# Kernel optimization log

Measured on AMD Instinct MI355X. Metric: run time of the kernel, lower is better.

## Reference

```python
import jax, jax.numpy as jnp
import numpy as np

EPS = 1e-5
M = 8          # num_modules
NUM_LAYERS = 4


def gumbel_softmax(logits, u, tau):
    g = -jnp.log(-jnp.log(jnp.clip(u, 1e-10, 1.0 - 1e-7)))
    return jax.nn.softmax((logits + g) / tau, axis=-1)


def batchnorm(x, gamma, beta):
    # training-mode BN over batch axis 0; x: [B, ...], gamma/beta broadcast over trailing dims
    mean = jnp.mean(x, axis=0, keepdims=True)
    var = jnp.mean(jnp.square(x - mean), axis=0, keepdims=True)  # biased var, as torch BN
    return (x - mean) * jax.lax.rsqrt(var + EPS) * gamma + beta


def setup_inputs() -> dict:
    key = jax.random.key(0)
    ks = jax.random.split(key, 32)
    B = 16384
    d = {}
    d['x'] = jax.random.normal(ks[0], (B, 128), jnp.float32)
    d['embedding_input'] = jax.random.normal(ks[1], (B, 128), jnp.float32)
    d['u_sel'] = jax.random.uniform(ks[2], (B, NUM_LAYERS - 1, M, M), jnp.float32)
    d['u_final'] = jax.random.uniform(ks[3], (B, M), jnp.float32)
    shapes = [('base_W0', (128, 400)), ('base_b0', (400,)), ('base_W1', (400, 256)), ('base_b1', (256,)),
              ('em_W0', (128, 400)), ('em_b0', (400,)),
              ('gat_W0', (400, 256)), ('gat_b0', (256,)), ('gat_W1', (256, 256)), ('gat_b1', (256,)),
              ('sel_W', (3, 256, 64)), ('sel_b', (3, 64)), ('selF_W', (256, 8)), ('selF_b', (8,)),
              ('cond_W', (3, 64, 256)), ('cond_b', (3, 256)),
              ('mod_W', (8, 256, 256)), ('mod_b', (8, 256)),
              ('last_W', (256, 18)), ('last_b', (18,))]
    for i, (name, sh) in enumerate(shapes):
        fan_in = sh[-2] if len(sh) >= 2 else sh[-1]
        d[name] = jax.random.normal(ks[4 + i], sh, jnp.float32) / np.sqrt(fan_in)
    d['bn1_g'] = jnp.ones((8, 256), jnp.float32)
    d['bn1_b'] = jnp.zeros((8, 256), jnp.float32)
    d['bn2_g'] = jnp.ones((8, 256), jnp.float32)
    d['bn2_b'] = jnp.zeros((8, 256), jnp.float32)
    return d


def forward(x, embedding_input, u_sel, u_final,
            base_W0, base_b0, base_W1, base_b1, em_W0, em_b0,
            gat_W0, gat_b0, gat_W1, gat_b1,
            sel_W, sel_b, selF_W, selF_b, cond_W, cond_b,
            mod_W, mod_b, bn1_g, bn1_b, bn2_g, bn2_b, last_W, last_b):
    relu = jax.nn.relu
    # base MLP (last activation is identity)
    h = relu(x @ base_W0 + base_b0)
    out = h @ base_W1 + base_b1                       # [B, 256]
    # embedding base (single layer, identity last activation)
    emb = embedding_input @ em_W0 + em_b0             # [B, 400]
    # gating fcs: activation THEN fc, per source loop
    emb = relu(emb) @ gat_W0 + gat_b0
    emb = relu(emb) @ gat_W1 + gat_b1                 # [B, 256]

    # routing logits (stochastic branch, tau = select_temp = 1.0)
    select_input = relu(emb)
    gsels = []
    for i in range(NUM_LAYERS - 1):
        logit = jnp.tanh(select_input @ sel_W[i] + sel_b[i])       # [B, 64]
        sraw = logit.reshape(logit.shape[0], M, M)                  # [B, M, M]
        gsels.append(gumbel_softmax(sraw, u_sel[:, i], 1.0))
        select_input = relu((logit @ cond_W[i] + cond_b[i]) * emb)
    final_select = gumbel_softmax(select_input @ selF_W + selF_b, u_final, 1.0)  # [B, M]
    # selects were insert(0, ...)'d in torch -> consumed in reversed order
    selects = gsels[::-1]

    # layer-0 expert modules: BN -> Linear -> BN (only layers[0] is used in forward)
    mean = jnp.mean(out, axis=0, keepdims=True)
    var = jnp.mean(jnp.square(out - mean), axis=0, keepdims=True)
    xhat = (out - mean) * jax.lax.rsqrt(var + EPS)                  # shared normalization
    t = xhat[:, None, :] * bn1_g + bn1_b                            # [B, M, 256] per-module affine
    h = jnp.einsum('bmd,mdh->bmh', t, mod_W) + mod_b                # [B, M, 256]
    prev = batchnorm(h, bn2_g, bn2_b)                               # [B, M, 256]

    # cascade: weighted combination + relu per layer
    for l in range(NUM_LAYERS - 1):
        prev = relu(jnp.einsum('bmk,bkh->bmh', selects[l], prev))
    out = jnp.einsum('bm,bmh->bh', final_select, prev)              # [B, 256]
    return out @ last_W + last_b                                    # [B, 18]


def reference(x, embedding_input, u_sel, u_final,
              base_W0, base_b0, base_W1, base_b1, em_W0, em_b0,
              gat_W0, gat_b0, gat_W1, gat_b1,
              sel_W, sel_b, selF_W, selF_b, cond_W, cond_b,
              mod_W, mod_b, bn1_g, bn1_b, bn2_g, bn2_b, last_W, last_b):
    return forward(x, embedding_input, u_sel, u_final,
                   base_W0, base_b0, base_W1, base_b1, em_W0, em_b0,
                   gat_W0, gat_b0, gat_W1, gat_b1,
                   sel_W, sel_b, selF_W, selF_b, cond_W, cond_b,
                   mod_W, mod_b, bn1_g, bn1_b, bn2_g, bn2_b, last_W, last_b)
```

## Files before the change

kernel.cpp:

```cpp
#include <hip/hip_runtime.h>
#include <math.h>


#define EPI_NONE  0
#define EPI_RELU  1
#define EPI_TANH  2
#define EPI_COND  3
#define EPI_STATS 4

typedef short bf16x8 __attribute__((ext_vector_type(8)));
typedef float f32x4 __attribute__((ext_vector_type(4)));

__device__ __forceinline__ unsigned short f2bf(float f) {
  unsigned u = __float_as_uint(f);
  u += 0x7fffu + ((u >> 16) & 1u);
  return (unsigned short)(u >> 16);
}
__device__ __forceinline__ float bf2f(unsigned short h) {
  return __uint_as_float(((unsigned)h) << 16);
}
__device__ __forceinline__ void gload_lds16(const void* g, void* l) {
  __builtin_amdgcn_global_load_lds(
      (const __attribute__((address_space(1))) unsigned int*)g,
      (__attribute__((address_space(3))) unsigned int*)l, 16, 0, 0);
}
__device__ __forceinline__ bf16x8 relu_bf8(bf16x8 v) {
  bf16x8 r;
  #pragma unroll
  for (int j = 0; j < 8; ++j) r[j] = v[j] > 0 ? v[j] : (short)0;
  return r;
}

__global__ __launch_bounds__(256) void prep_all(
    const float* __restrict__ x, const float* __restrict__ embi,
    const float* __restrict__ base_W0, const float* __restrict__ em_W0,
    const float* __restrict__ base_W1, const float* __restrict__ gat_W0,
    const float* __restrict__ gat_W1, const float* __restrict__ sel_W,
    const float* __restrict__ cond_W, const float* __restrict__ last_W,
    unsigned short* __restrict__ x_bf, unsigned short* __restrict__ e_bf,
    unsigned short* __restrict__ W0t, unsigned short* __restrict__ emW0t,
    unsigned short* __restrict__ W1t, unsigned short* __restrict__ g0t,
    unsigned short* __restrict__ g1t, unsigned short* __restrict__ selWt,
    unsigned short* __restrict__ condWt, unsigned short* __restrict__ lastWt,
    float* __restrict__ stats)
{
  __shared__ float t[32][33];
  int bid = blockIdx.x;
  const int tid = threadIdx.x;

  if (bid < 4096) {
    const float* src = bid < 2048 ? x : embi;
    unsigned short* dst = bid < 2048 ? x_bf : e_bf;
    const int i = ((bid & 2047) * 256 + tid) * 4;
    const float4 v = *reinterpret_cast<const float4*>(&src[i]);
    ushort4 o;
    o.x = f2bf(v.x); o.y = f2bf(v.y); o.z = f2bf(v.z); o.w = f2bf(v.w);
    *reinterpret_cast<ushort4*>(&dst[i]) = o;
    return;
  }
  bid -= 4096;

  const int tx = tid & 31, ty = tid >> 5;

  if (bid < 496) {
    const float* src; unsigned short* dst; int K, N, KP, gx, local;
    if (bid < 64)       { src = base_W0; dst = W0t;   K = 128; N = 400; KP = 128; gx = 4;  local = bid; }
    else if (bid < 128) { src = em_W0;   dst = emW0t; K = 128; N = 400; KP = 128; gx = 4;  local = bid - 64; }
    else if (bid < 232) { src = base_W1; dst = W1t;   K = 400; N = 256; KP = 416; gx = 13; local = bid - 128; }
    else if (bid < 336) { src = gat_W0;  dst = g0t;   K = 400; N = 256; KP = 416; gx = 13; local = bid - 232; }
    else if (bid < 400) { src = gat_W1;  dst = g1t;   K = 256; N = 256; KP = 256; gx = 8;  local = bid - 336; }
    else if (bid < 448) {
      const int i = (bid - 400) / 16;
      src = sel_W + i * 16384; dst = selWt + i * 16384;
      K = 256; N = 64; KP = 256; gx = 8; local = (bid - 400) % 16;
    } else {
      const int i = (bid - 448) / 16;
      src = cond_W + i * 16384; dst = condWt + i * 16384;
      K = 64; N = 256; KP = 64; gx = 2; local = (bid - 448) % 16;
    }
    const int k0 = (local % gx) * 32, n0 = (local / gx) * 32;
    #pragma unroll
    for (int p = 0; p < 4; ++p) {
      const int k = k0 + ty + p * 8;
      t[ty + p * 8][tx] = (k < K && n0 + tx < N) ? src[(size_t)k * N + n0 + tx] : 0.f;
    }
    __syncthreads();
    #pragma unroll
    for (int p = 0; p < 4; ++p) {
      const int n = n0 + ty + p * 8;
      dst[(size_t)n * KP + k0 + tx] = f2bf(t[tx][ty + p * 8]);
    }
    return;
  }
  bid -= 496;

  if (bid < 8) {
    const int k0 = bid * 32;
    #pragma unroll
    for (int p = 0; p < 4; ++p)
      t[ty + p * 8][tx] = (tx < 18) ? last_W[(size_t)(k0 + ty + p * 8) * 18 + tx] : 0.f;
    __syncthreads();
    #pragma unroll
    for (int p = 0; p < 4; ++p) {
      const int n = ty + p * 8;
      lastWt[(size_t)n * 256 + k0 + tx] = f2bf(t[tx][n]);
      lastWt[(size_t)(n + 32) * 256 + k0 + tx] = 0;
    }
    return;
  }

  for (int i = tid; i < 4608; i += 256) stats[i] = 0.f;
}

template<int BN, int WM, int WN, int EPI, bool RELU_A>
__global__ __launch_bounds__(256) void gemm_bf16(
    const unsigned short* __restrict__ A, int AS,
    const unsigned short* __restrict__ Wt, const float* __restrict__ bias,
    unsigned short* __restrict__ C, int CS, int Nreal, int NP, int K,
    const unsigned short* __restrict__ emb,
    float* __restrict__ sum, float* __restrict__ sumsq)
{
  constexpr int FRAG_M = 128 / WM / 16;
  constexpr int FRAG_N = BN / WN / 16;
  __shared__ unsigned short As[128 * 32];
  __shared__ unsigned short Bs[BN * 32];
  const int row0 = blockIdx.y * 128;
  const int n0 = blockIdx.x * BN;
  const int tid = threadIdx.x;
  const int wid = tid >> 6, lane = tid & 63;
  const int wr = wid / WN, wc = wid % WN;
  const int arow = tid >> 2;
  const int kcol = (tid & 3) * 8;
  const int lr = lane & 15, lk = (lane >> 4) * 8;
  const int lrow = (lane >> 4) * 4;

  f32x4 acc[FRAG_M][FRAG_N] = {};
  for (int k0 = 0; k0 < K; k0 += 32) {
    gload_lds16(A + (size_t)(row0 + arow) * AS + k0 + kcol, (char*)As + tid * 16);
    gload_lds16(A + (size_t)(row0 + 64 + arow) * AS + k0 + kcol, (char*)As + 4096 + tid * 16);
    gload_lds16(Wt + (size_t)(n0 + arow) * K + k0 + kcol, (char*)Bs + tid * 16);
    if constexpr (BN == 128)
      gload_lds16(Wt + (size_t)(n0 + 64 + arow) * K + k0 + kcol, (char*)Bs + 4096 + tid * 16);
    __syncthreads();
    bf16x8 a[FRAG_M], b[FRAG_N];
    #pragma unroll
    for (int i = 0; i < FRAG_M; ++i) {
      a[i] = *reinterpret_cast<const bf16x8*>(&As[(wr * (128 / WM) + i * 16 + lr) * 32 + lk]);
      if (RELU_A) a[i] = relu_bf8(a[i]);
    }
    #pragma unroll
    for (int j = 0; j < FRAG_N; ++j)
      b[j] = *reinterpret_cast<const bf16x8*>(&Bs[(wc * (BN / WN) + j * 16 + lr) * 32 + lk]);
    #pragma unroll
    for (int i = 0; i < FRAG_M; ++i)
      #pragma unroll
      for (int j = 0; j < FRAG_N; ++j)
        acc[i][j] = __builtin_amdgcn_mfma_f32_16x16x32_bf16(a[i], b[j], acc[i][j], 0, 0, 0);
    __syncthreads();
  }
  #pragma unroll
  for (int j = 0; j < FRAG_N; ++j) {
    const int col = n0 + wc * (BN / WN) + j * 16 + lr;
    if (col >= NP) continue;
    const bool real = col < Nreal;
    const float bv = real ? bias[col] : 0.f;
    float s = 0.f, q = 0.f;
    #pragma unroll
    for (int i = 0; i < FRAG_M; ++i) {
      #pragma unroll
      for (int r = 0; r < 4; ++r) {
        const int row = row0 + wr * (128 / WM) + i * 16 + lrow + r;
        float v = acc[i][j][r] + bv;
        if (EPI == EPI_RELU) v = fmaxf(v, 0.f);
        if (EPI == EPI_TANH) v = tanhf(v);
        if (EPI == EPI_COND) { v *= bf2f(emb[(size_t)row * 256 + col]); v = fmaxf(v, 0.f); }
        if (!real) v = 0.f;
        const unsigned short hv = f2bf(v);
        C[(size_t)row * CS + col] = hv;
        if (EPI == EPI_STATS) {
          const float vr = bf2f(hv);
          s += vr;
          q = fmaf(vr, vr, q);
        }
      }
    }
    if (EPI == EPI_STATS) {
      s += __shfl_xor(s, 16); s += __shfl_xor(s, 32);
      q += __shfl_xor(q, 16); q += __shfl_xor(q, 32);
      if (lane < 16) {
        atomicAdd(&sum[col], s);
        atomicAdd(&sumsq[col], q);
      }
    }
  }
}

__global__ __launch_bounds__(256) void gemm_last(
    const unsigned short* __restrict__ A, const unsigned short* __restrict__ Wt,
    const float* __restrict__ bias, float* __restrict__ out)
{
  __shared__ unsigned short As[128 * 32];
  __shared__ unsigned short Bs[64 * 32];
  const int row0 = blockIdx.y * 128;
  const int tid = threadIdx.x;
  const int wid = tid >> 6, lane = tid & 63;
  const int arow = tid >> 2;
  const int kcol = (tid & 3) * 8;
  const int lr = lane & 15, lk = (lane >> 4) * 8;
  const int lrow = (lane >> 4) * 4;

  f32x4 acc[2][4] = {};
  for (int k0 = 0; k0 < 256; k0 += 32) {
    gload_lds16(A + (size_t)(row0 + arow) * 256 + k0 + kcol, (char*)As + tid * 16);
    gload_lds16(A + (size_t)(row0 + 64 + arow) * 256 + k0 + kcol, (char*)As + 4096 + tid * 16);
    gload_lds16(Wt + (size_t)arow * 256 + k0 + kcol, (char*)Bs + tid * 16);
    __syncthreads();
    bf16x8 a[2], b[4];
    #pragma unroll
    for (int i = 0; i < 2; ++i)
      a[i] = *reinterpret_cast<const bf16x8*>(&As[(wid * 32 + i * 16 + lr) * 32 + lk]);
    #pragma unroll
    for (int j = 0; j < 4; ++j)
      b[j] = *reinterpret_cast<const bf16x8*>(&Bs[(j * 16 + lr) * 32 + lk]);
    #pragma unroll
    for (int i = 0; i < 2; ++i)
      #pragma unroll
      for (int j = 0; j < 4; ++j)
        acc[i][j] = __builtin_amdgcn_mfma_f32_16x16x32_bf16(a[i], b[j], acc[i][j], 0, 0, 0);
    __syncthreads();
  }
  #pragma unroll
  for (int j = 0; j < 2; ++j) {
    const int col = j * 16 + lr;
    if (col >= 18) continue;
    const float bv = bias[col];
    #pragma unroll
    for (int i = 0; i < 2; ++i) {
      #pragma unroll
      for (int r = 0; r < 4; ++r) {
        const int row = row0 + wid * 32 + i * 16 + lrow + r;
        out[(size_t)row * 18 + col] = acc[i][j][r] + bv;
      }
    }
  }
}

__global__ void gumbel8(const unsigned short* __restrict__ logit, const float* __restrict__ u,
                        float* __restrict__ out, int u_off, int u_stride)
{
  const int idx = blockIdx.x * 256 + threadIdx.x;
  const int b = idx >> 3, m = idx & 7;
  const unsigned short* lp = logit + (size_t)b * 64 + m * 8;
  const float* up = u + (size_t)b * u_stride + u_off + m * 8;
  float v[8];
  #pragma unroll
  for (int j = 0; j < 8; ++j) {
    const float uu = fminf(fmaxf(up[j], 1e-10f), 0.9999999f);
    v[j] = bf2f(lp[j]) - logf(-logf(uu));
  }
  float mx = v[0];
  #pragma unroll
  for (int j = 1; j < 8; ++j) mx = fmaxf(mx, v[j]);
  float s = 0.f;
  #pragma unroll
  for (int j = 0; j < 8; ++j) { v[j] = expf(v[j] - mx); s += v[j]; }
  const float inv = 1.f / s;
  float* op = out + (size_t)b * 64 + m * 8;
  #pragma unroll
  for (int j = 0; j < 8; ++j) op[j] = v[j] * inv;
}

__global__ void final_select_k(const unsigned short* __restrict__ si, const float* __restrict__ Wf,
                               const float* __restrict__ bias, const float* __restrict__ u,
                               float* __restrict__ fs)
{
  const int idx = blockIdx.x * 256 + threadIdx.x;
  const int b = idx >> 3, j = idx & 7;
  const unsigned short* sp = si + (size_t)b * 256;
  float acc = bias[j];
  for (int k = 0; k < 256; ++k) acc = fmaf(bf2f(sp[k]), Wf[k * 8 + j], acc);
  const float uu = fminf(fmaxf(u[(size_t)b * 8 + j], 1e-10f), 0.9999999f);
  float v = acc - logf(-logf(uu));
  float mx = v;
  #pragma unroll
  for (int d = 1; d < 8; d <<= 1) mx = fmaxf(mx, __shfl_xor(mx, d, 8));
  float e = expf(v - mx);
  float s = e;
  #pragma unroll
  for (int d = 1; d < 8; d <<= 1) s += __shfl_xor(s, d, 8);
  fs[(size_t)b * 8 + j] = e / s;
}

__global__ __launch_bounds__(256) void fold_modw_all(
    const float* __restrict__ W, const float* __restrict__ g1,
    const float* __restrict__ b1, const float* __restrict__ modb,
    const float* __restrict__ sum1, const float* __restrict__ sumsq1,
    unsigned short* __restrict__ Wt, float* __restrict__ bias2)
{
  const float invB = 1.f / 16384.f;
  if (blockIdx.z == 8) {
    if (blockIdx.y != 0) return;
    const int m = blockIdx.x, h = threadIdx.x;
    float acc = modb[m * 256 + h];
    for (int d = 0; d < 256; ++d) {
      const float mean = sum1[d] * invB;
      const float var = sumsq1[d] * invB - mean * mean;
      const float r = rsqrtf(var + 1e-5f);
      const float c = b1[m * 256 + d] - mean * r * g1[m * 256 + d];
      acc = fmaf(c, W[((size_t)m * 256 + d) * 256 + h], acc);
    }
    bias2[m * 256 + h] = acc;
    return;
  }
  __shared__ float t[32][33];
  const int m = blockIdx.z, d0 = blockIdx.y * 32, h0 = blockIdx.x * 32;
  const int tx = threadIdx.x & 31, ty = threadIdx.x >> 5;
  #pragma unroll
  for (int p = 0; p < 4; ++p) {
    const int d = d0 + ty + p * 8;
    const float mean = sum1[d] * invB;
    const float var = sumsq1[d] * invB - mean * mean;
    const float r = rsqrtf(var + 1e-5f);
    t[ty + p * 8][tx] = W[((size_t)m * 256 + d) * 256 + h0 + tx] * r * g1[m * 256 + d];
  }
  __syncthreads();
  #pragma unroll
  for (int p = 0; p < 4; ++p) {
    const int h = h0 + ty + p * 8;
    Wt[((size_t)m * 256 + h) * 256 + d0 + tx] = f2bf(t[tx][ty + p * 8]);
  }
}

__global__ void finalize_bn2(const float* __restrict__ sum, const float* __restrict__ sumsq,
                             const float* __restrict__ g, const float* __restrict__ b,
                             float* __restrict__ scale, float* __restrict__ shift)
{
  const int i = blockIdx.x * 256 + threadIdx.x;
  const float invB = 1.f / 16384.f;
  const float m = sum[i] * invB;
  const float v = sumsq[i] * invB - m * m;
  const float r = rsqrtf(v + 1e-5f);
  const float sc = r * g[i];
  scale[i] = sc;
  shift[i] = b[i] - m * sc;
}

__global__ __launch_bounds__(256) void final_cascade(
    const unsigned short* __restrict__ H, const float* __restrict__ scale2,
    const float* __restrict__ shift2, const float* __restrict__ gs0,
    const float* __restrict__ gs1, const float* __restrict__ gs2,
    const float* __restrict__ fs, unsigned short* __restrict__ ovec)
{
  const int wave = threadIdx.x >> 6, lane = threadIdx.x & 63;
  const int b = __builtin_amdgcn_readfirstlane(blockIdx.x * 4 + wave);
  const int c0 = lane << 2;

  float prev[8][4];
  #pragma unroll
  for (int m = 0; m < 8; ++m) {
    const int gc = m * 256 + c0;
    const ushort4 h = *reinterpret_cast<const ushort4*>(&H[(size_t)b * 2048 + gc]);
    const float4 sc = *reinterpret_cast<const float4*>(&scale2[gc]);
    const float4 sh = *reinterpret_cast<const float4*>(&shift2[gc]);
    prev[m][0] = bf2f(h.x) * sc.x + sh.x;
    prev[m][1] = bf2f(h.y) * sc.y + sh.y;
    prev[m][2] = bf2f(h.z) * sc.z + sh.z;
    prev[m][3] = bf2f(h.w) * sc.w + sh.w;
  }

  const float* sel0 = gs2 + (size_t)b * 64;
  const float* sel1 = gs1 + (size_t)b * 64;
  const float* sel2 = gs0 + (size_t)b * 64;
  #pragma unroll
  for (int l = 0; l < 3; ++l) {
    const float* sp = (l == 0) ? sel0 : (l == 1) ? sel1 : sel2;
    float nw[8][4];
    #pragma unroll
    for (int m = 0; m < 8; ++m) {
      float a0 = 0.f, a1 = 0.f, a2 = 0.f, a3 = 0.f;
      #pragma unroll
      for (int k = 0; k < 8; ++k) {
        const float s = sp[m * 8 + k];
        a0 = fmaf(s, prev[k][0], a0);
        a1 = fmaf(s, prev[k][1], a1);
        a2 = fmaf(s, prev[k][2], a2);
        a3 = fmaf(s, prev[k][3], a3);
      }
      nw[m][0] = fmaxf(a0, 0.f); nw[m][1] = fmaxf(a1, 0.f);
      nw[m][2] = fmaxf(a2, 0.f); nw[m][3] = fmaxf(a3, 0.f);
    }
    #pragma unroll
    for (int m = 0; m < 8; ++m)
      #pragma unroll
      for (int c = 0; c < 4; ++c)
        prev[m][c] = nw[m][c];
  }

  const float* fp = fs + (size_t)b * 8;
  float ov[4] = {0.f, 0.f, 0.f, 0.f};
  #pragma unroll
  for (int m = 0; m < 8; ++m) {
    const float s = fp[m];
    ov[0] = fmaf(s, prev[m][0], ov[0]);
    ov[1] = fmaf(s, prev[m][1], ov[1]);
    ov[2] = fmaf(s, prev[m][2], ov[2]);
    ov[3] = fmaf(s, prev[m][3], ov[3]);
  }
  ushort4 o;
  o.x = f2bf(ov[0]); o.y = f2bf(ov[1]); o.z = f2bf(ov[2]); o.w = f2bf(ov[3]);
  *reinterpret_cast<ushort4*>(&ovec[(size_t)b * 256 + c0]) = o;
}

extern "C" void kernel_launch(void* const* d_in, const int* in_sizes, int n_in,
                              void* d_out, int out_size, void* d_ws, size_t ws_size,
                              hipStream_t stream)
{
  (void)in_sizes; (void)n_in; (void)out_size; (void)ws_size;
  const float* x       = (const float*)d_in[0];
  const float* embi    = (const float*)d_in[1];
  const float* u_sel   = (const float*)d_in[2];
  const float* u_fin   = (const float*)d_in[3];
  const float* base_W0 = (const float*)d_in[4];
  const float* base_b0 = (const float*)d_in[5];
  const float* base_W1 = (const float*)d_in[6];
  const float* base_b1 = (const float*)d_in[7];
  const float* em_W0   = (const float*)d_in[8];
  const float* em_b0   = (const float*)d_in[9];
  const float* gat_W0  = (const float*)d_in[10];
  const float* gat_b0  = (const float*)d_in[11];
  const float* gat_W1  = (const float*)d_in[12];
  const float* gat_b1  = (const float*)d_in[13];
  const float* sel_W   = (const float*)d_in[14];
  const float* sel_b   = (const float*)d_in[15];
  const float* selF_W  = (const float*)d_in[16];
  const float* selF_b  = (const float*)d_in[17];
  const float* cond_W  = (const float*)d_in[18];
  const float* cond_b  = (const float*)d_in[19];
  const float* mod_W   = (const float*)d_in[20];
  const float* mod_b   = (const float*)d_in[21];
  const float* last_W  = (const float*)d_in[22];
  const float* last_b  = (const float*)d_in[23];
  const float* bn1_g   = (const float*)d_in[24];
  const float* bn1_b   = (const float*)d_in[25];
  const float* bn2_g   = (const float*)d_in[26];
  const float* bn2_b   = (const float*)d_in[27];

  char* WSB = (char*)d_ws;
  unsigned short* h_big    = (unsigned short*)(WSB + 0);
  unsigned short* h1       = (unsigned short*)(WSB + 67108864);
  unsigned short* ovec_bf  = (unsigned short*)(WSB + 67108864);
  unsigned short* x_bf     = (unsigned short*)(WSB + 80740352);
  unsigned short* e_bf     = (unsigned short*)(WSB + 84934656);
  unsigned short* emb_bf   = (unsigned short*)(WSB + 89128960);
  unsigned short* si_bf    = (unsigned short*)(WSB + 97517568);
  unsigned short* out_bf   = (unsigned short*)(WSB + 105906176);
  unsigned short* logit_bf = (unsigned short*)(WSB + 114294784);
  float* gs0   = (float*)(WSB + 116391936);
  float* gs1   = (float*)(WSB + 120586240);
  float* gs2   = (float*)(WSB + 124780544);
  float* bufFs = (float*)(WSB + 128974848);
  unsigned short* W0t   = (unsigned short*)(WSB + 129499136);
  unsigned short* emW0t = (unsigned short*)(WSB + 129630208);
  unsigned short* W1t   = (unsigned short*)(WSB + 129761280);
  unsigned short* g0t   = (unsigned short*)(WSB + 129974272);
  unsigned short* g1t   = (unsigned short*)(WSB + 130187264);
  unsigned short* selWt = (unsigned short*)(WSB + 130318336);
  unsigned short* condWt= (unsigned short*)(WSB + 130416640);
  unsigned short* modWt = (unsigned short*)(WSB + 130514944);
  float* bias2  = (float*)(WSB + 131563520);
  float* stats  = (float*)(WSB + 131571712);
  unsigned short* lastWt = (unsigned short*)(WSB + 131590144);
  float* scale2 = (float*)(WSB + 131622912);
  float* shift2 = (float*)(WSB + 131631104);
  float* sum1   = stats;        float* sumsq1 = stats + 256;
  float* sum2   = stats + 512;  float* sumsq2 = stats + 2560;

  const dim3 blk(256);
  prep_all<<<dim3(4601), blk, 0, stream>>>(
      x, embi, base_W0, em_W0, base_W1, gat_W0, gat_W1, sel_W, cond_W, last_W,
      x_bf, e_bf, W0t, emW0t, W1t, g0t, g1t, selWt, condWt, lastWt, stats);

  gemm_bf16<128, 2, 2, EPI_RELU, false><<<dim3(4, 128), blk, 0, stream>>>(
      x_bf, 128, W0t, base_b0, h1, 416, 400, 416, 128, nullptr, nullptr, nullptr);
  gemm_bf16<128, 2, 2, EPI_STATS, false><<<dim3(2, 128), blk, 0, stream>>>(
      h1, 416, W1t, base_b1, out_bf, 256, 256, 256, 416, nullptr, sum1, sumsq1);
  gemm_bf16<128, 2, 2, EPI_RELU, false><<<dim3(4, 128), blk, 0, stream>>>(
      e_bf, 128, emW0t, em_b0, h1, 416, 400, 416, 128, nullptr, nullptr, nullptr);
  gemm_bf16<128, 2, 2, EPI_RELU, false><<<dim3(2, 128), blk, 0, stream>>>(
      h1, 416, g0t, gat_b0, si_bf, 256, 256, 256, 416, nullptr, nullptr, nullptr);
  gemm_bf16<128, 2, 2, EPI_NONE, false><<<dim3(2, 128), blk, 0, stream>>>(
      si_bf, 256, g1t, gat_b1, emb_bf, 256, 256, 256, 256, nullptr, nullptr, nullptr);
  float* gs[3] = {gs0, gs1, gs2};
  for (int i = 0; i < 3; ++i) {
    if (i == 0)
      gemm_bf16<64, 4, 1, EPI_TANH, true><<<dim3(1, 128), blk, 0, stream>>>(
          emb_bf, 256, selWt, sel_b, logit_bf, 64, 64, 64, 256, nullptr, nullptr, nullptr);
    else
      gemm_bf16<64, 4, 1, EPI_TANH, false><<<dim3(1, 128), blk, 0, stream>>>(
          si_bf, 256, selWt + i * 16384, sel_b + i * 64, logit_bf, 64, 64, 64, 256, nullptr, nullptr, nullptr);
    gumbel8<<<dim3(512), blk, 0, stream>>>(logit_bf, u_sel, gs[i], i * 64, 192);
    gemm_bf16<128, 2, 2, EPI_COND, false><<<dim3(2, 128), blk, 0, stream>>>(
        logit_bf, 64, condWt + i * 16384, cond_b + i * 256, si_bf, 256, 256, 256, 64, emb_bf, nullptr, nullptr);
  }
  final_select_k<<<dim3(512), blk, 0, stream>>>(si_bf, selF_W, selF_b, u_fin, bufFs);
  fold_modw_all<<<dim3(8, 8, 9), blk, 0, stream>>>(
      mod_W, bn1_g, bn1_b, mod_b, sum1, sumsq1, modWt, bias2);
  gemm_bf16<128, 2, 2, EPI_STATS, false><<<dim3(16, 128), blk, 0, stream>>>(
      out_bf, 256, modWt, bias2, h_big, 2048, 2048, 2048, 256, nullptr, sum2, sumsq2);
  finalize_bn2<<<dim3(8), blk, 0, stream>>>(sum2, sumsq2, bn2_g, bn2_b, scale2, shift2);
  final_cascade<<<dim3(4096), blk, 0, stream>>>(
      h_big, scale2, shift2, gs0, gs1, gs2, bufFs, ovec_bf);
  gemm_last<<<dim3(1, 128), blk, 0, stream>>>(ovec_bf, lastWt, last_b, (float*)d_out);
}
```

Baseline: 268.0 us.

## Batch the two first-layer GEMMs and add a fragment-layout module GEMM

The x and embedding first-layer GEMMs now run as one launch using blockIdx.z, with separate h1 buffers so both outputs can coexist. The big per-module GEMM moves to a new kernel that reads weights pre-shuffled into MFMA fragment order straight from global memory instead of through LDS. A swizzle on the A tile is meant to avoid LDS bank conflicts, and the output is staged in LDS so it can be written with 16-byte stores. This costs an extra reshuffle kernel and a larger workspace.

```diff
diff --git a/kernel.cpp b/kernel.cpp
--- a/kernel.cpp
+++ b/kernel.cpp
@@ -118,12 +118,18 @@
     const unsigned short* __restrict__ Wt, const float* __restrict__ bias,
     unsigned short* __restrict__ C, int CS, int Nreal, int NP, int K,
     const unsigned short* __restrict__ emb,
-    float* __restrict__ sum, float* __restrict__ sumsq)
+    float* __restrict__ sum, float* __restrict__ sumsq,
+    const unsigned short* A2, const unsigned short* W2,
+    const float* bias_b, unsigned short* C2)
 {
   constexpr int FRAG_M = 128 / WM / 16;
   constexpr int FRAG_N = BN / WN / 16;
   __shared__ unsigned short As[128 * 32];
   __shared__ unsigned short Bs[BN * 32];
+  const unsigned short* Ap = (blockIdx.z == 0) ? A : A2;
+  const unsigned short* Wp = (blockIdx.z == 0) ? Wt : W2;
+  const float* bp = (blockIdx.z == 0) ? bias : bias_b;
+  unsigned short* Cp = (blockIdx.z == 0) ? C : C2;
   const int row0 = blockIdx.y * 128;
   const int n0 = blockIdx.x * BN;
   const int tid = threadIdx.x;
@@ -136,11 +142,11 @@
 
   f32x4 acc[FRAG_M][FRAG_N] = {};
   for (int k0 = 0; k0 < K; k0 += 32) {
-    gload_lds16(A + (size_t)(row0 + arow) * AS + k0 + kcol, (char*)As + tid * 16);
-    gload_lds16(A + (size_t)(row0 + 64 + arow) * AS + k0 + kcol, (char*)As + 4096 + tid * 16);
-    gload_lds16(Wt + (size_t)(n0 + arow) * K + k0 + kcol, (char*)Bs + tid * 16);
+    gload_lds16(Ap + (size_t)(row0 + arow) * AS + k0 + kcol, (char*)As + tid * 16);
+    gload_lds16(Ap + (size_t)(row0 + 64 + arow) * AS + k0 + kcol, (char*)As + 4096 + tid * 16);
+    gload_lds16(Wp + (size_t)(n0 + arow) * K + k0 + kcol, (char*)Bs + tid * 16);
     if constexpr (BN == 128)
-      gload_lds16(Wt + (size_t)(n0 + 64 + arow) * K + k0 + kcol, (char*)Bs + 4096 + tid * 16);
+      gload_lds16(Wp + (size_t)(n0 + 64 + arow) * K + k0 + kcol, (char*)Bs + 4096 + tid * 16);
     __syncthreads();
     bf16x8 a[FRAG_M], b[FRAG_N];
     #pragma unroll
@@ -163,7 +169,7 @@
     const int col = n0 + wc * (BN / WN) + j * 16 + lr;
     if (col >= NP) continue;
     const bool real = col < Nreal;
-    const float bv = real ? bias[col] : 0.f;
+    const float bv = real ? bp[col] : 0.f;
     float s = 0.f, q = 0.f;
     #pragma unroll
     for (int i = 0; i < FRAG_M; ++i) {
@@ -176,7 +182,7 @@
         if (EPI == EPI_COND) { v *= bf2f(emb[(size_t)row * 256 + col]); v = fmaxf(v, 0.f); }
         if (!real) v = 0.f;
         const unsigned short hv = f2bf(v);
-        C[(size_t)row * CS + col] = hv;
+        Cp[(size_t)row * CS + col] = hv;
         if (EPI == EPI_STATS) {
           const float vr = bf2f(hv);
           s += vr;
@@ -195,52 +201,87 @@
   }
 }
 
-__global__ __launch_bounds__(256) void gemm_last(
-    const unsigned short* __restrict__ A, const unsigned short* __restrict__ Wt,
-    const float* __restrict__ bias, float* __restrict__ out)
+__global__ __launch_bounds__(256) void gemm_mod_frag(
+    const unsigned short* __restrict__ Abf,
+    const unsigned short* __restrict__ Wt2,
+    const float* __restrict__ bias2,
+    unsigned short* __restrict__ H,
+    float* __restrict__ sum, float* __restrict__ sumsq)
 {
   __shared__ unsigned short As[128 * 32];
-  __shared__ unsigned short Bs[64 * 32];
-  const int row0 = blockIdx.y * 128;
+  __shared__ unsigned short Cs[128 * 136];
   const int tid = threadIdx.x;
   const int wid = tid >> 6, lane = tid & 63;
+  const int wr = wid >> 1, wc = wid & 1;
+  const int lr = lane & 15, hi = lane >> 4;
+  const int m = blockIdx.x >> 1, half = blockIdx.x & 1;
+  const int row0 = blockIdx.y * 128;
   const int arow = tid >> 2;
-  const int kcol = (tid & 3) * 8;
-  const int lr = lane & 15, lk = (lane >> 4) * 8;
-  const int lrow = (lane >> 4) * 4;
-
-  f32x4 acc[2][4] = {};
-  for (int k0 = 0; k0 < 256; k0 += 32) {
-    gload_lds16(A + (size_t)(row0 + arow) * 256 + k0 + kcol, (char*)As + tid * 16);
-    gload_lds16(A + (size_t)(row0 + 64 + arow) * 256 + k0 + kcol, (char*)As + 4096 + tid * 16);
-    gload_lds16(Wt + (size_t)arow * 256 + k0 + kcol, (char*)Bs + tid * 16);
-    __syncthreads();
-    bf16x8 a[2], b[4];
-    #pragma unroll
-    for (int i = 0; i < 2; ++i)
-      a[i] = *reinterpret_cast<const bf16x8*>(&As[(wid * 32 + i * 16 + lr) * 32 + lk]);
-    #pragma unroll
-    for (int j = 0; j < 4; ++j)
-      b[j] = *reinterpret_cast<const bf16x8*>(&Bs[(j * 16 + lr) * 32 + lk]);
-    #pragma unroll
-    for (int i = 0; i < 2; ++i)
+  const int cg = (tid & 3) ^ (arow & 3);
+
+  f32x4 acc[4][4] = {};
+  for (int ks = 0; ks < 8; ++ks) {
+    const int k0 = ks * 32;
+    __syncthreads();
+    gload_lds16(Abf + (size_t)(row0 + arow) * 256 + k0 + cg * 8, (char*)As + tid * 16);
+    gload_lds16(Abf + (size_t)(row0 + 64 + arow) * 256 + k0 + cg * 8,
+                (char*)As + 4096 + tid * 16);
+    __syncthreads();
+    bf16x8 a[4], b[4];
+    #pragma unroll
+    for (int i = 0; i < 4; ++i) {
+      const int row = wr * 64 + i * 16 + lr;
+      a[i] = *reinterpret_cast<const bf16x8*>(
+          (const char*)As + row * 64 + ((hi ^ (lr & 3)) * 16));
+    }
+    #pragma unroll
+    for (int j = 0; j < 4; ++j) {
+      const int J = half * 8 + wc * 4 + j;
+      b[j] = *reinterpret_cast<const bf16x8*>(
+          Wt2 + (size_t)((m * 16 + J) * 8 + ks) * 512 + lane * 8);
+    }
+    #pragma unroll
+    for (int i = 0; i < 4; ++i)
       #pragma unroll
       for (int j = 0; j < 4; ++j)
         acc[i][j] = __builtin_amdgcn_mfma_f32_16x16x32_bf16(a[i], b[j], acc[i][j], 0, 0, 0);
-    __syncthreads();
-  }
-  #pragma unroll
-  for (int j = 0; j < 2; ++j) {
-    const int col = j * 16 + lr;
-    if (col >= 18) continue;
-    const float bv = bias[col];
-    #pragma unroll
-    for (int i = 0; i < 2; ++i) {
+  }
+
+  __syncthreads();
+  #pragma unroll
+  for (int j = 0; j < 4; ++j) {
+    const int J = half * 8 + wc * 4 + j;
+    const int gc = m * 256 + J * 16 + lr;
+    const float bv = bias2[gc];
+    float s = 0.f, q = 0.f;
+    #pragma unroll
+    for (int i = 0; i < 4; ++i) {
       #pragma unroll
       for (int r = 0; r < 4; ++r) {
-        const int row = row0 + wid * 32 + i * 16 + lrow + r;
-        out[(size_t)row * 18 + col] = acc[i][j][r] + bv;
+        const unsigned short hv = f2bf(acc[i][j][r] + bv);
+        Cs[(wr * 64 + i * 16 + hi * 4 + r) * 136 + wc * 64 + j * 16 + lr] = hv;
+        const float vr = bf2f(hv);
+        s += vr;
+        q = fmaf(vr, vr, q);
       }
+    }
+    s += __shfl_xor(s, 16); s += __shfl_xor(s, 32);
+    q += __shfl_xor(q, 16); q += __shfl_xor(q, 32);
+    if (lane < 16) {
+      atomicAdd(&sum[gc], s);
+      atomicAdd(&sumsq[gc], q);
+    }
+  }
+  __syncthreads();
+  const int colbase = m * 256 + half * 128;
+  #pragma unroll
+  for (int pass = 0; pass < 2; ++pass) {
+    const int row = pass * 64 + (tid >> 2);
+    const int qc = (tid & 3) * 32;
+    #pragma unroll
+    for (int v = 0; v < 4; ++v) {
+      const uint4 d = *reinterpret_cast<const uint4*>(&Cs[row * 136 + qc + v * 8]);
+      *reinterpret_cast<uint4*>(&H[(size_t)(row0 + row) * 2048 + colbase + qc + v * 8]) = d;
     }
   }
 }
@@ -331,6 +372,18 @@
   }
 }
 
+__global__ __launch_bounds__(256) void reshuffle_w(
+    const unsigned short* __restrict__ modWt, unsigned short* __restrict__ Wt2)
+{
+  const int idx = blockIdx.x * 256 + threadIdx.x;
+  const int ks = idx & 7, col = (idx >> 3) & 255, m = idx >> 11;
+  const unsigned short* src = modWt + ((size_t)m * 256 + col) * 256 + ks * 32;
+  unsigned short* dst = Wt2 + (size_t)((m * 16 + (col >> 4)) * 8 + ks) * 512 + (col & 15) * 8;
+  #pragma unroll
+  for (int h2 = 0; h2 < 4; ++h2)
+    *reinterpret_cast<uint4*>(dst + h2 * 128) = *reinterpret_cast<const uint4*>(src + h2 * 8);
+}
+
 __global__ void finalize_bn2(const float* __restrict__ sum, const float* __restrict__ sumsq,
                              const float* __restrict__ g, const float* __restrict__ b,
                              float* __restrict__ scale, float* __restrict__ shift)
@@ -409,6 +462,56 @@
   ushort4 o;
   o.x = f2bf(ov[0]); o.y = f2bf(ov[1]); o.z = f2bf(ov[2]); o.w = f2bf(ov[3]);
   *reinterpret_cast<ushort4*>(&ovec[(size_t)b * 256 + c0]) = o;
+}
+
+__global__ __launch_bounds__(256) void gemm_last(
+    const unsigned short* __restrict__ A, const unsigned short* __restrict__ Wt,
+    const float* __restrict__ bias, float* __restrict__ out)
+{
+  __shared__ unsigned short As[128 * 32];
+  __shared__ unsigned short Bs[64 * 32];
+  const int row0 = blockIdx.y * 128;
+  const int tid = threadIdx.x;
+  const int wid = tid >> 6, lane = tid & 63;
+  const int arow = tid >> 2;
+  const int kcol = (tid & 3) * 8;
+  const int lr = lane & 15, lk = (lane >> 4) * 8;
+  const int lrow = (lane >> 4) * 4;
+
+  f32x4 acc[2][4] = {};
+  for (int k0 = 0; k0 < 256; k0 += 32) {
+    gload_lds16(A + (size_t)(row0 + arow) * 256 + k0 + kcol, (char*)As + tid * 16);
+    gload_lds16(A + (size_t)(row0 + 64 + arow) * 256 + k0 + kcol, (char*)As + 4096 + tid * 16);
+    gload_lds16(Wt + (size_t)arow * 256 + k0 + kcol, (char*)Bs + tid * 16);
+    __syncthreads();
+    bf16x8 a[2], b[4];
+    #pragma unroll
+    for (int i = 0; i < 2; ++i)
+      a[i] = *reinterpret_cast<const bf16x8*>(&As[(wid * 32 + i * 16 + lr) * 32 + lk]);
+    #pragma unroll
+    for (int j = 0; j < 4; ++j)
+      b[j] = *reinterpret_cast<const bf16x8*>(&Bs[(j * 16 + lr) * 32 + lk]);
+    #pragma unroll
+    for (int i = 0; i < 2; ++i)
+      #pragma unroll
+      for (int j = 0; j < 4; ++j)
+        acc[i][j] = __builtin_amdgcn_mfma_f32_16x16x32_bf16(a[i], b[j], acc[i][j], 0, 0, 0);
+    __syncthreads();
+  }
+  #pragma unroll
+  for (int j = 0; j < 2; ++j) {
+    const int col = j * 16 + lr;
+    if (col >= 18) continue;
+    const float bv = bias[col];
+    #pragma unroll
+    for (int i = 0; i < 2; ++i) {
+      #pragma unroll
+      for (int r = 0; r < 4; ++r) {
+        const int row = row0 + wid * 32 + i * 16 + lrow + r;
+        out[(size_t)row * 18 + col] = acc[i][j][r] + bv;
+      }
+    }
+  }
 }
 
 extern "C" void kernel_launch(void* const* d_in, const int* in_sizes, int n_in,
@@ -447,31 +550,33 @@
 
   char* WSB = (char*)d_ws;
   unsigned short* h_big    = (unsigned short*)(WSB + 0);
-  unsigned short* h1       = (unsigned short*)(WSB + 67108864);
+  unsigned short* h1e      = (unsigned short*)(WSB + 67108864);
   unsigned short* ovec_bf  = (unsigned short*)(WSB + 67108864);
-  unsigned short* x_bf     = (unsigned short*)(WSB + 80740352);
-  unsigned short* e_bf     = (unsigned short*)(WSB + 84934656);
-  unsigned short* emb_bf   = (unsigned short*)(WSB + 89128960);
-  unsigned short* si_bf    = (unsigned short*)(WSB + 97517568);
-  unsigned short* out_bf   = (unsigned short*)(WSB + 105906176);
-  unsigned short* logit_bf = (unsigned short*)(WSB + 114294784);
-  float* gs0   = (float*)(WSB + 116391936);
-  float* gs1   = (float*)(WSB + 120586240);
-  float* gs2   = (float*)(WSB + 124780544);
-  float* bufFs = (float*)(WSB + 128974848);
-  unsigned short* W0t   = (unsigned short*)(WSB + 129499136);
-  unsigned short* emW0t = (unsigned short*)(WSB + 129630208);
-  unsigned short* W1t   = (unsigned short*)(WSB + 129761280);
-  unsigned short* g0t   = (unsigned short*)(WSB + 129974272);
-  unsigned short* g1t   = (unsigned short*)(WSB + 130187264);
-  unsigned short* selWt = (unsigned short*)(WSB + 130318336);
-  unsigned short* condWt= (unsigned short*)(WSB + 130416640);
-  unsigned short* modWt = (unsigned short*)(WSB + 130514944);
-  float* bias2  = (float*)(WSB + 131563520);
-  float* stats  = (float*)(WSB + 131571712);
-  unsigned short* lastWt = (unsigned short*)(WSB + 131590144);
-  float* scale2 = (float*)(WSB + 131622912);
-  float* shift2 = (float*)(WSB + 131631104);
+  unsigned short* h1       = (unsigned short*)(WSB + 81000448);
+  unsigned short* x_bf     = (unsigned short*)(WSB + 94631936);
+  unsigned short* e_bf     = (unsigned short*)(WSB + 98826240);
+  unsigned short* emb_bf   = (unsigned short*)(WSB + 103020544);
+  unsigned short* si_bf    = (unsigned short*)(WSB + 111409152);
+  unsigned short* out_bf   = (unsigned short*)(WSB + 119797760);
+  unsigned short* logit_bf = (unsigned short*)(WSB + 128186368);
+  float* gs0   = (float*)(WSB + 130283520);
+  float* gs1   = (float*)(WSB + 134477824);
+  float* gs2   = (float*)(WSB + 138672128);
+  float* bufFs = (float*)(WSB + 142866432);
+  unsigned short* W0t   = (unsigned short*)(WSB + 143390720);
+  unsigned short* emW0t = (unsigned short*)(WSB + 143521792);
+  unsigned short* W1t   = (unsigned short*)(WSB + 143652864);
+  unsigned short* g0t   = (unsigned short*)(WSB + 143865856);
+  unsigned short* g1t   = (unsigned short*)(WSB + 144078848);
+  unsigned short* selWt = (unsigned short*)(WSB + 144209920);
+  unsigned short* condWt= (unsigned short*)(WSB + 144308224);
+  unsigned short* modWt = (unsigned short*)(WSB + 144406528);
+  unsigned short* Wt2   = (unsigned short*)(WSB + 145455104);
+  float* bias2  = (float*)(WSB + 146503680);
+  float* stats  = (float*)(WSB + 146511872);
+  unsigned short* lastWt = (unsigned short*)(WSB + 146530304);
+  float* scale2 = (float*)(WSB + 146563072);
+  float* shift2 = (float*)(WSB + 146571264);
   float* sum1   = stats;        float* sumsq1 = stats + 256;
   float* sum2   = stats + 512;  float* sumsq2 = stats + 2560;
 
@@ -480,33 +585,39 @@
       x, embi, base_W0, em_W0, base_W1, gat_W0, gat_W1, sel_W, cond_W, last_W,
       x_bf, e_bf, W0t, emW0t, W1t, g0t, g1t, selWt, condWt, lastWt, stats);
 
-  gemm_bf16<128, 2, 2, EPI_RELU, false><<<dim3(4, 128), blk, 0, stream>>>(
-      x_bf, 128, W0t, base_b0, h1, 416, 400, 416, 128, nullptr, nullptr, nullptr);
+  gemm_bf16<128, 2, 2, EPI_RELU, false><<<dim3(4, 128, 2), blk, 0, stream>>>(
+      x_bf, 128, W0t, base_b0, h1, 416, 400, 416, 128, nullptr, nullptr, nullptr,
+      e_bf, emW0t, em_b0, h1e);
   gemm_bf16<128, 2, 2, EPI_STATS, false><<<dim3(2, 128), blk, 0, stream>>>(
-      h1, 416, W1t, base_b1, out_bf, 256, 256, 256, 416, nullptr, sum1, sumsq1);
-  gemm_bf16<128, 2, 2, EPI_RELU, false><<<dim3(4, 128), blk, 0, stream>>>(
-      e_bf, 128, emW0t, em_b0, h1, 416, 400, 416, 128, nullptr, nullptr, nullptr);
+      h1, 416, W1t, base_b1, out_bf, 256, 256, 256, 416, nullptr, sum1, sumsq1,
+      nullptr, nullptr, nullptr, nullptr);
   gemm_bf16<128, 2, 2, EPI_RELU, false><<<dim3(2, 128), blk, 0, stream>>>(
-      h1, 416, g0t, gat_b0, si_bf, 256, 256, 256, 416, nullptr, nullptr, nullptr);
+      h1e, 416, g0t, gat_b0, si_bf, 256, 256, 256, 416, nullptr, nullptr, nullptr,
+      nullptr, nullptr, nullptr, nullptr);
   gemm_bf16<128, 2, 2, EPI_NONE, false><<<dim3(2, 128), blk, 0, stream>>>(
-      si_bf, 256, g1t, gat_b1, emb_bf, 256, 256, 256, 256, nullptr, nullptr, nullptr);
+      si_bf, 256, g1t, gat_b1, emb_bf, 256, 256, 256, 256, nullptr, nullptr, nullptr,
+      nullptr, nullptr, nullptr, nullptr);
   float* gs[3] = {gs0, gs1, gs2};
   for (int i = 0; i < 3; ++i) {
     if (i == 0)
       gemm_bf16<64, 4, 1, EPI_TANH, true><<<dim3(1, 128), blk, 0, stream>>>(
-          emb_bf, 256, selWt, sel_b, logit_bf, 64, 64, 64, 256, nullptr, nullptr, nullptr);
+          emb_bf, 256, selWt, sel_b, logit_bf, 64, 64, 64, 256, nullptr, nullptr, nullptr,
+          nullptr, nullptr, nullptr, nullptr);
     else
       gemm_bf16<64, 4, 1, EPI_TANH, false><<<dim3(1, 128), blk, 0, stream>>>(
-          si_bf, 256, selWt + i * 16384, sel_b + i * 64, logit_bf, 64, 64, 64, 256, nullptr, nullptr, nullptr);
+          si_bf, 256, selWt + i * 16384, sel_b + i * 64, logit_bf, 64, 64, 64, 256,
+          nullptr, nullptr, nullptr, nullptr, nullptr, nullptr, nullptr);
     gumbel8<<<dim3(512), blk, 0, stream>>>(logit_bf, u_sel, gs[i], i * 64, 192);
     gemm_bf16<128, 2, 2, EPI_COND, false><<<dim3(2, 128), blk, 0, stream>>>(
-        logit_bf, 64, condWt + i * 16384, cond_b + i * 256, si_bf, 256, 256, 256, 64, emb_bf, nullptr, nullptr);
+        logit_bf, 64, condWt + i * 16384, cond_b + i * 256, si_bf, 256, 256, 256, 64,
+        emb_bf, nullptr, nullptr, nullptr, nullptr, nullptr, nullptr);
   }
   final_select_k<<<dim3(512), blk, 0, stream>>>(si_bf, selF_W, selF_b, u_fin, bufFs);
   fold_modw_all<<<dim3(8, 8, 9), blk, 0, stream>>>(
       mod_W, bn1_g, bn1_b, mod_b, sum1, sumsq1, modWt, bias2);
-  gemm_bf16<128, 2, 2, EPI_STATS, false><<<dim3(16, 128), blk, 0, stream>>>(
-      out_bf, 256, modWt, bias2, h_big, 2048, 2048, 2048, 256, nullptr, sum2, sumsq2);
+  reshuffle_w<<<dim3(64), blk, 0, stream>>>(modWt, Wt2);
+  gemm_mod_frag<<<dim3(16, 128), blk, 0, stream>>>(
+      out_bf, Wt2, bias2, h_big, sum2, sumsq2);
   finalize_bn2<<<dim3(8), blk, 0, stream>>>(sum2, sumsq2, bn2_g, bn2_b, scale2, shift2);
   final_cascade<<<dim3(4096), blk, 0, stream>>>(
       h_big, scale2, shift2, gs0, gs1, gs2, bufFs, ovec_bf);
```

Result: slower. 296.1 us (+10.5%).
